# Optimization experiments

Measured on AMD Instinct MI355X. Metric: run time of the kernel, lower is better.

The kernel has to match this reference:

```python
import jax, jax.numpy as jnp
import numpy as np

BT, L, F, N = 8, 8192, 128, 16


def setup_inputs() -> dict:
    key = jax.random.key(0)
    ks = jax.random.split(key, 7)
    scale = 1.0 / np.sqrt(F)
    x = jax.random.normal(ks[0], (BT, L, F), dtype=jnp.float32)
    Wb = jax.random.normal(ks[1], (F, N), dtype=jnp.float32) * scale
    bb = jax.random.normal(ks[2], (N,), dtype=jnp.float32) * 0.01
    Wc = jax.random.normal(ks[3], (F, N), dtype=jnp.float32) * scale
    bc = jax.random.normal(ks[4], (N,), dtype=jnp.float32) * 0.01
    Wd = jax.random.normal(ks[5], (F, 1), dtype=jnp.float32) * scale
    bd = jax.random.normal(ks[6], (1,), dtype=jnp.float32) * 0.01
    # diagonal HiPPO-like spectrum (A is diagonal in the source: torch.diag(eigenvalues))
    A = -(jnp.arange(N, dtype=jnp.float32) + 1.0)
    return {"x": x, "Wb": Wb, "bb": bb, "Wc": Wc, "bc": bc, "Wd": Wd, "bd": bd, "A": A}


def reference(x, Wb, bb, Wc, bc, Wd, bd, A):
    # input-dependent SSM parameters (S6 / selective scan)
    B = x @ Wb + bb                      # [BT, L, N]
    C = x @ Wc + bc                      # [BT, L, N]
    delta = jax.nn.softplus(x @ Wd + bd)  # [BT, L, 1]
    # ZOH discretization with diagonal A
    dA = jnp.exp(delta * A)              # [BT, L, N]
    dB = (dA - 1.0) / A * B              # [BT, L, N]

    def step(h, inp):
        dA_t, dB_t, x_t, C_t = inp       # [BT,N],[BT,N],[BT,F],[BT,N]
        # h: [BT, F, N]; each feature channel has its own N-dim state
        h = dA_t[:, None, :] * h + dB_t[:, None, :] * x_t[:, :, None]
        y = jnp.einsum('bfn,bn->bf', h, C_t)
        return h, y

    h0 = jnp.zeros((x.shape[0], x.shape[2], A.shape[0]), dtype=x.dtype)
    xs = (jnp.swapaxes(dA, 0, 1), jnp.swapaxes(dB, 0, 1),
          jnp.swapaxes(x, 0, 1), jnp.swapaxes(C, 0, 1))
    _, ys = jax.lax.scan(step, h0, xs)   # ys: [L, BT, F]
    return jnp.swapaxes(ys, 0, 1)        # [BT, L, F]
```

## Files before the change

kernel.cpp:

```cpp
#include <hip/hip_runtime.h>
#include <hip/hip_bf16.h>


#define BTc   8
#define Lseq  8192
#define Fdim  128
#define Ndim  16
#define CH    128
#define LC    64

__device__ inline uint32_t pkbf(float a, float b) {
    union { __hip_bfloat162 h; uint32_t u; } cv;
    cv.h.x = __float2bfloat16(a);
    cv.h.y = __float2bfloat16(b);
    return cv.u;
}
__device__ inline void upbf(uint32_t u, float& lo, float& hi) {
    union { uint32_t i; float f; } a, b;
    a.i = u << 16; b.i = u & 0xffff0000u;
    lo = a.f; hi = b.f;
}

__global__ __launch_bounds__(256) void k_pre(
    const float* __restrict__ x,
    const float* __restrict__ Wb, const float* __restrict__ bb,
    const float* __restrict__ Wc, const float* __restrict__ bc,
    const float* __restrict__ Wd, const float* __restrict__ bd,
    const float* __restrict__ A,  uint32_t* __restrict__ G,
    float* __restrict__ E, float* __restrict__ S)
{
    __shared__ float Wl[33][4][36];
    __shared__ float Dl[2][64];
    __shared__ float Cum[2][64];
    const int tid = threadIdx.x;
    for (int idx = tid; idx < 33 * 128; idx += 256) {
        int j = idx >> 7, k = idx & 127;
        float v;
        if (j < 16)      v = Wb[k * 16 + j];
        else if (j < 32) v = Wc[k * 16 + (j - 16)];
        else             v = Wd[k];
        Wl[j][k >> 5][k & 31] = v;
    }
    __syncthreads();

    const int t2 = tid >> 2, ks = tid & 3;
    const size_t gtok0 = (size_t)blockIdx.x * 128;
    const size_t tokA = gtok0 + t2;
    const float4* xA = reinterpret_cast<const float4*>(x + tokA * 128 + ks * 32);
    const float4* xB = reinterpret_cast<const float4*>(x + (tokA + 64) * 128 + ks * 32);

    float accA[33], accB[33];
#pragma unroll
    for (int j = 0; j < 33; ++j) { accA[j] = 0.f; accB[j] = 0.f; }

#pragma unroll 2
    for (int kk = 0; kk < 8; ++kk) {
        float4 a = xA[kk], b = xB[kk];
#pragma unroll
        for (int j = 0; j < 33; ++j) {
            float4 w = *reinterpret_cast<const float4*>(&Wl[j][ks][kk * 4]);
            accA[j] = fmaf(a.x, w.x, accA[j]);
            accA[j] = fmaf(a.y, w.y, accA[j]);
            accA[j] = fmaf(a.z, w.z, accA[j]);
            accA[j] = fmaf(a.w, w.w, accA[j]);
            accB[j] = fmaf(b.x, w.x, accB[j]);
            accB[j] = fmaf(b.y, w.y, accB[j]);
            accB[j] = fmaf(b.z, w.z, accB[j]);
            accB[j] = fmaf(b.w, w.w, accB[j]);
        }
    }

    float sel[33];
#pragma unroll
    for (int j = 0; j < 33; ++j) {
        accA[j] += __shfl_xor(accA[j], 1);
        accA[j] += __shfl_xor(accA[j], 2);
        accB[j] += __shfl_xor(accB[j], 1);
        accB[j] += __shfl_xor(accB[j], 2);
        sel[j] = (ks & 1) ? accB[j] : accA[j];
    }

    float Cv[16];
    if (ks < 2) {
        const size_t tok = gtok0 + (size_t)ks * 64 + t2;
        float v = sel[32] + bd[0];
        float delta = fmaxf(v, 0.f) + log1pf(expf(-fabsf(v)));
        Dl[ks][t2] = delta;
        float out[48];
#pragma unroll
        for (int n = 0; n < 16; ++n) {
            float An = A[n];
            float dA = expf(delta * An);
            Cv[n] = sel[16 + n] + bc[n];
            out[n]      = dA;
            out[16 + n] = (dA - 1.f) / An * (sel[n] + bb[n]);
            out[32 + n] = Cv[n];
        }
        uint32_t gw[24];
#pragma unroll
        for (int p = 0; p < 24; ++p) gw[p] = pkbf(out[2*p], out[2*p+1]);
        uint4* Gr = reinterpret_cast<uint4*>(G + tok * 24);
#pragma unroll
        for (int p = 0; p < 6; ++p)
            Gr[p] = make_uint4(gw[4*p], gw[4*p+1], gw[4*p+2], gw[4*p+3]);
    }
    __syncthreads();

    if (tid < 128) {
        const int w = tid >> 6, lane = tid & 63;
        float cum = Dl[w][lane];
#pragma unroll
        for (int off = 1; off < 64; off <<= 1) {
            float up = __shfl_up(cum, off);
            cum += (lane >= off) ? up : 0.f;
        }
        Cum[w][lane] = cum;
        if (lane == 63) S[blockIdx.x * 2 + w] = cum;
    }
    __syncthreads();

    if (ks < 2) {
        const size_t chunk = (size_t)blockIdx.x * 2 + ks;
        float cumv = Cum[ks][t2];
        float Ev[16];
#pragma unroll
        for (int n = 0; n < 16; ++n)
            Ev[n] = Cv[n] * expf(A[n] * cumv);
        float4* Ep = reinterpret_cast<float4*>(E + (chunk * 64 + t2) * 16);
#pragma unroll
        for (int p = 0; p < 4; ++p)
            Ep[p] = make_float4(Ev[4*p], Ev[4*p+1], Ev[4*p+2], Ev[4*p+3]);
    }
}

__global__ __launch_bounds__(128) void k_scan(
    const float* __restrict__ x, const uint32_t* __restrict__ G,
    float* __restrict__ y, float* __restrict__ q)
{
    __shared__ float    Xl[LC][Fdim];
    __shared__ uint32_t Gl[LC][24];
    const int c = blockIdx.x, b = blockIdx.y;
    const int f = threadIdx.x;
    const size_t tok0 = (size_t)b * Lseq + (size_t)c * LC;

    const float4* xg = reinterpret_cast<const float4*>(x + tok0 * Fdim);
    float4* xs = reinterpret_cast<float4*>(&Xl[0][0]);
    for (int i = f; i < LC * Fdim / 4; i += 128) xs[i] = xg[i];
    const uint4* gg = reinterpret_cast<const uint4*>(G + tok0 * 24);
    uint4* gs = reinterpret_cast<uint4*>(&Gl[0][0]);
    for (int i = f; i < LC * 6; i += 128) gs[i] = gg[i];
    __syncthreads();

    float h[16];
#pragma unroll
    for (int n = 0; n < 16; ++n) h[n] = 0.f;

    float* yp = y + tok0 * Fdim + f;
#pragma unroll 4
    for (int t = 0; t < LC; ++t) {
        float xv = Xl[t][f];
        const uint4* gp = reinterpret_cast<const uint4*>(&Gl[t][0]);
        uint4 g0 = gp[0], g1 = gp[1], g2 = gp[2], g3 = gp[3], g4 = gp[4], g5 = gp[5];
        float da[16], db[16], cc[16];
        upbf(g0.x, da[0], da[1]);  upbf(g0.y, da[2],  da[3]);
        upbf(g0.z, da[4], da[5]);  upbf(g0.w, da[6],  da[7]);
        upbf(g1.x, da[8], da[9]);  upbf(g1.y, da[10], da[11]);
        upbf(g1.z, da[12], da[13]); upbf(g1.w, da[14], da[15]);
        upbf(g2.x, db[0], db[1]);  upbf(g2.y, db[2],  db[3]);
        upbf(g2.z, db[4], db[5]);  upbf(g2.w, db[6],  db[7]);
        upbf(g3.x, db[8], db[9]);  upbf(g3.y, db[10], db[11]);
        upbf(g3.z, db[12], db[13]); upbf(g3.w, db[14], db[15]);
        upbf(g4.x, cc[0], cc[1]);  upbf(g4.y, cc[2],  cc[3]);
        upbf(g4.z, cc[4], cc[5]);  upbf(g4.w, cc[6],  cc[7]);
        upbf(g5.x, cc[8], cc[9]);  upbf(g5.y, cc[10], cc[11]);
        upbf(g5.z, cc[12], cc[13]); upbf(g5.w, cc[14], cc[15]);
        float yacc = 0.f;
#pragma unroll
        for (int n = 0; n < 16; ++n) {
            h[n] = fmaf(da[n], h[n], db[n] * xv);
            yacc = fmaf(cc[n], h[n], yacc);
        }
        yp[t * Fdim] = yacc;
    }

    float4* qp = reinterpret_cast<float4*>(q + ((size_t)(b * CH + c) * Fdim + f) * 16);
#pragma unroll
    for (int p = 0; p < 4; ++p)
        qp[p] = make_float4(h[4*p], h[4*p+1], h[4*p+2], h[4*p+3]);
}

__global__ __launch_bounds__(256) void k_chunkscan(
    const float* __restrict__ q, const float* __restrict__ S,
    const float* __restrict__ A, float* __restrict__ Hin)
{
    int id = blockIdx.x * 256 + threadIdx.x;
    int b  = id >> 11;
    int fn = id & 2047;
    int n  = id & 15;
    float An = A[n];
    float H = 0.f;
    size_t qb = (size_t)b * CH * 2048 + fn;
    const float* Sb = S + b * CH;
    for (int cg = 0; cg < CH; cg += 16) {
        float Sr[16], qr[16];
#pragma unroll
        for (int i = 0; i < 16; ++i) {
            Sr[i] = Sb[cg + i];
            qr[i] = q[qb + (size_t)(cg + i) * 2048];
        }
#pragma unroll
        for (int i = 0; i < 16; ++i) {
            Hin[qb + (size_t)(cg + i) * 2048] = H;
            H = fmaf(__expf(An * Sr[i]), H, qr[i]);
        }
    }
}

__global__ __launch_bounds__(128) void k_correct(
    const float* __restrict__ Hin, const float* __restrict__ E,
    float* __restrict__ y)
{
    __shared__ float El[LC][16];
    const int c = blockIdx.x, b = blockIdx.y;
    const int f = threadIdx.x;

    const float4* Eg = reinterpret_cast<const float4*>(E + (size_t)(b * CH + c) * LC * 16);
    float4* Es = reinterpret_cast<float4*>(&El[0][0]);
    for (int i = f; i < LC * 4; i += 128) Es[i] = Eg[i];

    float hv[16];
    const float4* hp = reinterpret_cast<const float4*>(Hin + ((size_t)(b * CH + c) * Fdim + f) * 16);
#pragma unroll
    for (int p = 0; p < 4; ++p) {
        float4 t4 = hp[p];
        hv[4*p] = t4.x; hv[4*p+1] = t4.y; hv[4*p+2] = t4.z; hv[4*p+3] = t4.w;
    }
    __syncthreads();

    float* yp = y + ((size_t)b * Lseq + (size_t)c * LC) * Fdim + f;
#pragma unroll 4
    for (int t = 0; t < LC; ++t) {
        const float4* ep = reinterpret_cast<const float4*>(&El[t][0]);
        float acc = 0.f;
#pragma unroll
        for (int p = 0; p < 4; ++p) {
            float4 e4 = ep[p];
            acc = fmaf(e4.x, hv[4*p],     acc);
            acc = fmaf(e4.y, hv[4*p + 1], acc);
            acc = fmaf(e4.z, hv[4*p + 2], acc);
            acc = fmaf(e4.w, hv[4*p + 3], acc);
        }
        yp[t * Fdim] += acc;
    }
}

extern "C" void kernel_launch(void* const* d_in, const int* in_sizes, int n_in,
                              void* d_out, int out_size, void* d_ws, size_t ws_size,
                              hipStream_t stream) {
    const float* x  = (const float*)d_in[0];
    const float* Wb = (const float*)d_in[1];
    const float* bb = (const float*)d_in[2];
    const float* Wc = (const float*)d_in[3];
    const float* bc = (const float*)d_in[4];
    const float* Wd = (const float*)d_in[5];
    const float* bd = (const float*)d_in[6];
    const float* A  = (const float*)d_in[7];
    float* y = (float*)d_out;

    uint32_t* G = (uint32_t*)d_ws;
    float* q    = (float*)(G + (size_t)BTc * Lseq * 24);
    float* Hin  = q   + (size_t)BTc * CH * Fdim * Ndim;
    float* E    = Hin + (size_t)BTc * CH * Fdim * Ndim;
    float* S    = E   + (size_t)BTc * Lseq * Ndim;

    k_pre<<<dim3(512), 256, 0, stream>>>(x, Wb, bb, Wc, bc, Wd, bd, A, G, E, S);
    k_scan<<<dim3(CH, BTc), 128, 0, stream>>>(x, G, y, q);
    k_chunkscan<<<dim3(BTc * Fdim * Ndim / 256), 256, 0, stream>>>(q, S, A, Hin);
    k_correct<<<dim3(CH, BTc), 128, 0, stream>>>(Hin, E, y);
}
```

Baseline: 90.66 us.

## Replace intra-chunk sequential scan with masked decay-matrix formulation (SSD style)

The per-chunk recurrent scan over 64 tokens is replaced by building a 64x64 lower-triangular mixing matrix M[t][s] = sum_n C_t,n dB_s,n exp(A_n (cum_t - cum_s)), then computing y and the chunk-final state as matrix-vector products against x held in registers. The E factors move from k_pre into k_correct, and G is stored as fp32 dB and C (dA dropped) instead of packed bf16. This removes the serial dependency chain in the scan and exposes more parallelism (256 threads per block). In exchange it adds exp2 work for the matrix, roughly 64 registers of x per thread, and a larger fp32 workspace footprint.

```diff
diff --git a/kernel.cpp b/kernel.cpp
--- a/kernel.cpp
+++ b/kernel.cpp
@@ -1,5 +1,4 @@
 #include <hip/hip_runtime.h>
-#include <hip/hip_bf16.h>
 
 
 #define BTc   8
@@ -8,26 +7,15 @@
 #define Ndim  16
 #define CH    128
 #define LC    64
-
-__device__ inline uint32_t pkbf(float a, float b) {
-    union { __hip_bfloat162 h; uint32_t u; } cv;
-    cv.h.x = __float2bfloat16(a);
-    cv.h.y = __float2bfloat16(b);
-    return cv.u;
-}
-__device__ inline void upbf(uint32_t u, float& lo, float& hi) {
-    union { uint32_t i; float f; } a, b;
-    a.i = u << 16; b.i = u & 0xffff0000u;
-    lo = a.f; hi = b.f;
-}
+#define LOG2E 1.44269504089f
 
 __global__ __launch_bounds__(256) void k_pre(
     const float* __restrict__ x,
     const float* __restrict__ Wb, const float* __restrict__ bb,
     const float* __restrict__ Wc, const float* __restrict__ bc,
     const float* __restrict__ Wd, const float* __restrict__ bd,
-    const float* __restrict__ A,  uint32_t* __restrict__ G,
-    float* __restrict__ E, float* __restrict__ S)
+    const float* __restrict__ A,  float* __restrict__ G,
+    float* __restrict__ cumG, float* __restrict__ S)
 {
     __shared__ float Wl[33][4][36];
     __shared__ float Dl[2][64];
@@ -80,29 +68,23 @@
         sel[j] = (ks & 1) ? accB[j] : accA[j];
     }
 
-    float Cv[16];
     if (ks < 2) {
         const size_t tok = gtok0 + (size_t)ks * 64 + t2;
         float v = sel[32] + bd[0];
         float delta = fmaxf(v, 0.f) + log1pf(expf(-fabsf(v)));
         Dl[ks][t2] = delta;
-        float out[48];
+        float out[32];
 #pragma unroll
         for (int n = 0; n < 16; ++n) {
             float An = A[n];
             float dA = expf(delta * An);
-            Cv[n] = sel[16 + n] + bc[n];
-            out[n]      = dA;
-            out[16 + n] = (dA - 1.f) / An * (sel[n] + bb[n]);
-            out[32 + n] = Cv[n];
-        }
-        uint32_t gw[24];
-#pragma unroll
-        for (int p = 0; p < 24; ++p) gw[p] = pkbf(out[2*p], out[2*p+1]);
-        uint4* Gr = reinterpret_cast<uint4*>(G + tok * 24);
-#pragma unroll
-        for (int p = 0; p < 6; ++p)
-            Gr[p] = make_uint4(gw[4*p], gw[4*p+1], gw[4*p+2], gw[4*p+3]);
+            out[n]      = (dA - 1.f) / An * (sel[n] + bb[n]);
+            out[16 + n] = sel[16 + n] + bc[n];
+        }
+        float4* Gr = reinterpret_cast<float4*>(G + tok * 32);
+#pragma unroll
+        for (int p = 0; p < 8; ++p)
+            Gr[p] = make_float4(out[4*p], out[4*p+1], out[4*p+2], out[4*p+3]);
     }
     __syncthreads();
 
@@ -118,75 +100,119 @@
         if (lane == 63) S[blockIdx.x * 2 + w] = cum;
     }
     __syncthreads();
-
-    if (ks < 2) {
-        const size_t chunk = (size_t)blockIdx.x * 2 + ks;
-        float cumv = Cum[ks][t2];
-        float Ev[16];
-#pragma unroll
-        for (int n = 0; n < 16; ++n)
-            Ev[n] = Cv[n] * expf(A[n] * cumv);
-        float4* Ep = reinterpret_cast<float4*>(E + (chunk * 64 + t2) * 16);
-#pragma unroll
-        for (int p = 0; p < 4; ++p)
-            Ep[p] = make_float4(Ev[4*p], Ev[4*p+1], Ev[4*p+2], Ev[4*p+3]);
-    }
-}
-
-__global__ __launch_bounds__(128) void k_scan(
-    const float* __restrict__ x, const uint32_t* __restrict__ G,
+    if (tid < 128) cumG[gtok0 + tid] = Cum[tid >> 6][tid & 63];
+}
+
+__global__ __launch_bounds__(256, 3) void k_ymm(
+    const float* __restrict__ x, const float* __restrict__ G,
+    const float* __restrict__ cumG, const float* __restrict__ S,
+    const float* __restrict__ A,
     float* __restrict__ y, float* __restrict__ q)
 {
-    __shared__ float    Xl[LC][Fdim];
-    __shared__ uint32_t Gl[LC][24];
+    __shared__ float Gt[LC][36];
+    __shared__ float argT[LC][16];
+    __shared__ float Mt[LC][68];
+    __shared__ float Fq[16][68];
+    __shared__ float cumL[LC];
+    __shared__ float A2l[16];
+
+    const int tid = threadIdx.x;
     const int c = blockIdx.x, b = blockIdx.y;
-    const int f = threadIdx.x;
     const size_t tok0 = (size_t)b * Lseq + (size_t)c * LC;
 
-    const float4* xg = reinterpret_cast<const float4*>(x + tok0 * Fdim);
-    float4* xs = reinterpret_cast<float4*>(&Xl[0][0]);
-    for (int i = f; i < LC * Fdim / 4; i += 128) xs[i] = xg[i];
-    const uint4* gg = reinterpret_cast<const uint4*>(G + tok0 * 24);
-    uint4* gs = reinterpret_cast<uint4*>(&Gl[0][0]);
-    for (int i = f; i < LC * 6; i += 128) gs[i] = gg[i];
-    __syncthreads();
-
-    float h[16];
-#pragma unroll
-    for (int n = 0; n < 16; ++n) h[n] = 0.f;
-
-    float* yp = y + tok0 * Fdim + f;
-#pragma unroll 4
-    for (int t = 0; t < LC; ++t) {
-        float xv = Xl[t][f];
-        const uint4* gp = reinterpret_cast<const uint4*>(&Gl[t][0]);
-        uint4 g0 = gp[0], g1 = gp[1], g2 = gp[2], g3 = gp[3], g4 = gp[4], g5 = gp[5];
-        float da[16], db[16], cc[16];
-        upbf(g0.x, da[0], da[1]);  upbf(g0.y, da[2],  da[3]);
-        upbf(g0.z, da[4], da[5]);  upbf(g0.w, da[6],  da[7]);
-        upbf(g1.x, da[8], da[9]);  upbf(g1.y, da[10], da[11]);
-        upbf(g1.z, da[12], da[13]); upbf(g1.w, da[14], da[15]);
-        upbf(g2.x, db[0], db[1]);  upbf(g2.y, db[2],  db[3]);
-        upbf(g2.z, db[4], db[5]);  upbf(g2.w, db[6],  db[7]);
-        upbf(g3.x, db[8], db[9]);  upbf(g3.y, db[10], db[11]);
-        upbf(g3.z, db[12], db[13]); upbf(g3.w, db[14], db[15]);
-        upbf(g4.x, cc[0], cc[1]);  upbf(g4.y, cc[2],  cc[3]);
-        upbf(g4.z, cc[4], cc[5]);  upbf(g4.w, cc[6],  cc[7]);
-        upbf(g5.x, cc[8], cc[9]);  upbf(g5.y, cc[10], cc[11]);
-        upbf(g5.z, cc[12], cc[13]); upbf(g5.w, cc[14], cc[15]);
-        float yacc = 0.f;
-#pragma unroll
-        for (int n = 0; n < 16; ++n) {
-            h[n] = fmaf(da[n], h[n], db[n] * xv);
-            yacc = fmaf(cc[n], h[n], yacc);
-        }
-        yp[t * Fdim] = yacc;
-    }
-
-    float4* qp = reinterpret_cast<float4*>(q + ((size_t)(b * CH + c) * Fdim + f) * 16);
-#pragma unroll
-    for (int p = 0; p < 4; ++p)
-        qp[p] = make_float4(h[4*p], h[4*p+1], h[4*p+2], h[4*p+3]);
+    {
+        const float4* Gg = reinterpret_cast<const float4*>(G + tok0 * 32);
+        for (int i = tid; i < 512; i += 256) {
+            int t = i >> 3, p = i & 7;
+            *reinterpret_cast<float4*>(&Gt[t][p * 4]) = Gg[i];
+        }
+        if (tid < 64) cumL[tid] = cumG[tok0 + tid];
+        if (tid < 16) A2l[tid] = A[tid] * LOG2E;
+    }
+    const int f = tid & 127;
+    float X[64];
+    {
+        const float* xp = x + tok0 * Fdim + f;
+#pragma unroll
+        for (int s = 0; s < 64; ++s) X[s] = xp[s * Fdim];
+    }
+    const float Sc = S[b * CH + c];
+    __syncthreads();
+
+    for (int i = tid; i < 1024; i += 256) {
+        int t = i >> 4, n = i & 15;
+        argT[t][n] = A2l[n] * cumL[t];
+    }
+    for (int i = tid; i < 1024; i += 256) {
+        int nn = i >> 6, s = i & 63;
+        Fq[nn][s] = Gt[s][nn] * exp2f(A2l[nn] * (Sc - cumL[s]));
+    }
+    __syncthreads();
+
+    {
+        const int s = tid & 63;
+        const int w = tid >> 6;
+        float dBs[16], args[16];
+#pragma unroll
+        for (int n = 0; n < 16; ++n) { dBs[n] = Gt[s][n]; args[n] = argT[s][n]; }
+        for (int k = 0; k < 16; ++k) {
+            int t = 4 * k + w;
+            const float4* Ct = reinterpret_cast<const float4*>(&Gt[t][16]);
+            const float4* at = reinterpret_cast<const float4*>(&argT[t][0]);
+            float acc = 0.f;
+#pragma unroll
+            for (int p = 0; p < 4; ++p) {
+                float4 c4 = Ct[p], a4 = at[p];
+                acc = fmaf(c4.x * dBs[4*p],   exp2f(a4.x - args[4*p]),   acc);
+                acc = fmaf(c4.y * dBs[4*p+1], exp2f(a4.y - args[4*p+1]), acc);
+                acc = fmaf(c4.z * dBs[4*p+2], exp2f(a4.z - args[4*p+2]), acc);
+                acc = fmaf(c4.w * dBs[4*p+3], exp2f(a4.w - args[4*p+3]), acc);
+            }
+            Mt[t][s] = (s <= t) ? acc : 0.f;
+        }
+    }
+    __syncthreads();
+
+    {
+        const int h = tid >> 7;
+        float* yp = y + tok0 * Fdim + f;
+#pragma unroll
+        for (int k = 0; k < 32; ++k) {
+            const int ns4 = ((2 * k + 1) >> 2) + 1;
+            int t = 2 * k + h;
+            const float4* Mrow = reinterpret_cast<const float4*>(&Mt[t][0]);
+            float a0 = 0.f, a1 = 0.f, a2 = 0.f, a3 = 0.f;
+#pragma unroll
+            for (int s4 = 0; s4 < ns4; ++s4) {
+                float4 m4 = Mrow[s4];
+                a0 = fmaf(m4.x, X[4*s4],     a0);
+                a1 = fmaf(m4.y, X[4*s4 + 1], a1);
+                a2 = fmaf(m4.z, X[4*s4 + 2], a2);
+                a3 = fmaf(m4.w, X[4*s4 + 3], a3);
+            }
+            yp[t * Fdim] = (a0 + a1) + (a2 + a3);
+        }
+        float4* qp = reinterpret_cast<float4*>(q + ((size_t)(b * CH + c) * Fdim + f) * 16 + h * 8);
+#pragma unroll
+        for (int nb = 0; nb < 2; ++nb) {
+            float qv[4];
+#pragma unroll
+            for (int j = 0; j < 4; ++j) {
+                const float4* Fr = reinterpret_cast<const float4*>(&Fq[h * 8 + nb * 4 + j][0]);
+                float b0 = 0.f, b1 = 0.f, b2 = 0.f, b3 = 0.f;
+#pragma unroll
+                for (int s4 = 0; s4 < 16; ++s4) {
+                    float4 f4 = Fr[s4];
+                    b0 = fmaf(f4.x, X[4*s4],     b0);
+                    b1 = fmaf(f4.y, X[4*s4 + 1], b1);
+                    b2 = fmaf(f4.z, X[4*s4 + 2], b2);
+                    b3 = fmaf(f4.w, X[4*s4 + 3], b3);
+                }
+                qv[j] = (b0 + b1) + (b2 + b3);
+            }
+            qp[nb] = make_float4(qv[0], qv[1], qv[2], qv[3]);
+        }
+    }
 }
 
 __global__ __launch_bounds__(256) void k_chunkscan(
@@ -217,16 +243,17 @@
 }
 
 __global__ __launch_bounds__(128) void k_correct(
-    const float* __restrict__ Hin, const float* __restrict__ E,
+    const float* __restrict__ G, const float* __restrict__ cumG,
+    const float* __restrict__ A, const float* __restrict__ Hin,
     float* __restrict__ y)
 {
     __shared__ float El[LC][16];
+    __shared__ float cumL[LC];
     const int c = blockIdx.x, b = blockIdx.y;
     const int f = threadIdx.x;
-
-    const float4* Eg = reinterpret_cast<const float4*>(E + (size_t)(b * CH + c) * LC * 16);
-    float4* Es = reinterpret_cast<float4*>(&El[0][0]);
-    for (int i = f; i < LC * 4; i += 128) Es[i] = Eg[i];
+    const size_t tok0 = (size_t)b * Lseq + (size_t)c * LC;
+
+    if (f < 64) cumL[f] = cumG[tok0 + f];
 
     float hv[16];
     const float4* hp = reinterpret_cast<const float4*>(Hin + ((size_t)(b * CH + c) * Fdim + f) * 16);
@@ -237,7 +264,14 @@
     }
     __syncthreads();
 
-    float* yp = y + ((size_t)b * Lseq + (size_t)c * LC) * Fdim + f;
+    for (int i = f; i < 1024; i += 128) {
+        int t = i >> 4, n = i & 15;
+        float A2n = A[n] * LOG2E;
+        El[t][n] = G[(tok0 + t) * 32 + 16 + n] * exp2f(A2n * cumL[t]);
+    }
+    __syncthreads();
+
+    float* yp = y + tok0 * Fdim + f;
 #pragma unroll 4
     for (int t = 0; t < LC; ++t) {
         const float4* ep = reinterpret_cast<const float4*>(&El[t][0]);
@@ -267,14 +301,14 @@
     const float* A  = (const float*)d_in[7];
     float* y = (float*)d_out;
 
-    uint32_t* G = (uint32_t*)d_ws;
-    float* q    = (float*)(G + (size_t)BTc * Lseq * 24);
-    float* Hin  = q   + (size_t)BTc * CH * Fdim * Ndim;
-    float* E    = Hin + (size_t)BTc * CH * Fdim * Ndim;
-    float* S    = E   + (size_t)BTc * Lseq * Ndim;
-
-    k_pre<<<dim3(512), 256, 0, stream>>>(x, Wb, bb, Wc, bc, Wd, bd, A, G, E, S);
-    k_scan<<<dim3(CH, BTc), 128, 0, stream>>>(x, G, y, q);
+    float* G    = (float*)d_ws;
+    float* q    = G    + (size_t)BTc * Lseq * 32;
+    float* Hin  = q    + (size_t)BTc * CH * Fdim * Ndim;
+    float* cumG = Hin  + (size_t)BTc * CH * Fdim * Ndim;
+    float* S    = cumG + (size_t)BTc * Lseq;
+
+    k_pre<<<dim3(512), 256, 0, stream>>>(x, Wb, bb, Wc, bc, Wd, bd, A, G, cumG, S);
+    k_ymm<<<dim3(CH, BTc), 256, 0, stream>>>(x, G, cumG, S, A, y, q);
     k_chunkscan<<<dim3(BTc * Fdim * Ndim / 256), 256, 0, stream>>>(q, S, A, Hin);
-    k_correct<<<dim3(CH, BTc), 128, 0, stream>>>(Hin, E, y);
-}
+    k_correct<<<dim3(CH, BTc), 128, 0, stream>>>(G, cumG, A, Hin, y);
+}
```

Measured after the change: 161.3 us. 1.78x slower.
